# Performance work log

Measured on AMD Instinct MI355X. Metric: run time of the kernel, lower is better.

Reference implementation:

```python
import jax, jax.numpy as jnp
import numpy as np

B = 65536      # batch of (state, action) pairs
DIM_S = 64     # input feature dim
DIM_C = 8      # number of options / experts
H = 256        # hidden width (two hidden layers)


def setup_inputs() -> dict:
    key = jax.random.key(0)
    ks = jax.random.split(key, 7)
    s = 0.05  # small init scale
    st = jax.random.normal(ks[0], (B, DIM_S), dtype=jnp.float32)
    # Batched expert weights: one slice per expert (dim_c experts).
    W1 = jax.random.normal(ks[1], (DIM_C, DIM_S, H), dtype=jnp.float32) * s
    b1 = jax.random.normal(ks[2], (DIM_C, H), dtype=jnp.float32) * s
    W2 = jax.random.normal(ks[3], (DIM_C, H, H), dtype=jnp.float32) * s
    b2 = jax.random.normal(ks[4], (DIM_C, H), dtype=jnp.float32) * s
    W3 = jax.random.normal(ks[5], (DIM_C, H, 1), dtype=jnp.float32) * s
    b3 = jax.random.normal(ks[6], (DIM_C, 1), dtype=jnp.float32) * s
    return {"st": st, "W1": W1, "b1": b1, "W2": W2, "b2": b2,
            "W3": W3, "b3": b3}


def reference(st, W1, b1, W2, b2, W3, b3):
    # Equivalent of torch.stack([m(st) for m in self.discriminator], dim=1):
    # every expert MLP (dim_s -> H -> H -> 1, ReLU) applied to the same st,
    # expressed as batched GEMMs over the expert axis c.
    h = jax.nn.relu(jnp.einsum('bs,csh->bch', st, W1) + b1[None])   # [B, C, H]
    h = jax.nn.relu(jnp.einsum('bch,chk->bck', h, W2) + b2[None])   # [B, C, H]
    d = jnp.einsum('bch,cho->bco', h, W3) + b3[None]                # [B, C, 1]
    return d
```

## Files before the change

kernel.cpp:

```cpp
#include <hip/hip_runtime.h>
#include <hip/hip_bf16.h>

typedef __bf16 bf16x8 __attribute__((ext_vector_type(8)));
typedef float  f32x4  __attribute__((ext_vector_type(4)));

static constexpr int S  = 64;
static constexpr int C  = 8;
static constexpr int HD = 256;

__device__ __forceinline__ unsigned short f2bf(float f) {
  __hip_bfloat16 b = __float2bfloat16(f);
  unsigned short u;
  __builtin_memcpy(&u, &b, 2);
  return u;
}

__device__ __forceinline__ void gl2lds16(const void* g, void* l) {
  __builtin_amdgcn_global_load_lds(
      (const __attribute__((address_space(1))) unsigned int*)g,
      (__attribute__((address_space(3))) unsigned int*)l, 16, 0, 0);
}

__global__ __launch_bounds__(256) void prep_weights(
    const float* __restrict__ W1, const float* __restrict__ W2,
    unsigned short* __restrict__ W1T, unsigned short* __restrict__ W2T)
{
  __shared__ float tile[32][33];
  const int tid = threadIdx.x, cl = tid & 31, r0 = tid >> 5;
  const int b = blockIdx.x;
  if (b < 512) {
    const int c = b >> 6, t = b & 63, kt = t >> 3, nt = t & 7;
    const float* src = W2 + c * 65536;
    #pragma unroll
    for (int i = 0; i < 4; ++i) {
      int r = r0 + 8 * i;
      tile[r][cl] = src[(kt * 32 + r) * 256 + nt * 32 + cl];
    }
    __syncthreads();
    unsigned short* dst = W2T + c * 65536;
    #pragma unroll
    for (int i = 0; i < 4; ++i) {
      int r = r0 + 8 * i;
      dst[(nt * 32 + r) * 256 + kt * 32 + cl] = f2bf(tile[cl][r]);
    }
  } else {
    const int bb = b - 512;
    const int c = bb >> 4, t = bb & 15, st2 = t >> 3, ht = t & 7;
    const float* src = W1 + c * 16384;
    #pragma unroll
    for (int i = 0; i < 4; ++i) {
      int r = r0 + 8 * i;
      tile[r][cl] = src[(st2 * 32 + r) * 256 + ht * 32 + cl];
    }
    __syncthreads();
    unsigned short* dst = W1T + c * 16384;
    #pragma unroll
    for (int i = 0; i < 4; ++i) {
      int r = r0 + 8 * i;
      dst[(ht * 32 + r) * 64 + st2 * 32 + cl] = f2bf(tile[cl][r]);
    }
  }
}

__global__ __launch_bounds__(256, 2) void moe_fused(
    const float* __restrict__ st,
    const unsigned short* __restrict__ W1T,
    const unsigned short* __restrict__ W2T,
    const float* __restrict__ b1,
    const float* __restrict__ b2,
    const float* __restrict__ W3,
    const float* __restrict__ b3,
    float* __restrict__ out)
{
  constexpr int LDT = 72;

  __shared__ __align__(16) unsigned short sT[256 * LDT];
  __shared__ __align__(16) unsigned short sW2[2 * 32 * 256];

  const int tid  = threadIdx.x;
  const int lane = tid & 63;
  const int wv   = tid >> 6;
  const int l15  = lane & 15;
  const int q    = lane >> 4;
  const int c    = blockIdx.x >> 8;
  const int row0 = (blockIdx.x & 255) * 256;

  const unsigned short* W1c = W1T + c * HD * S;
  const unsigned short* W2c = W2T + c * HD * HD;

  bf16x8 aA[4][2];
  #pragma unroll
  for (int nt = 0; nt < 4; ++nt)
    #pragma unroll
    for (int ks = 0; ks < 2; ++ks) {
      const int row = row0 + wv * 64 + nt * 16 + l15;
      const float4* p = reinterpret_cast<const float4*>(st + (size_t)row * S + ks * 32 + q * 8);
      float4 x = p[0], y = p[1];
      union { bf16x8 v; unsigned short u[8]; } a;
      a.u[0] = f2bf(x.x); a.u[1] = f2bf(x.y); a.u[2] = f2bf(x.z); a.u[3] = f2bf(x.w);
      a.u[4] = f2bf(y.x); a.u[5] = f2bf(y.y); a.u[6] = f2bf(y.z); a.u[7] = f2bf(y.w);
      aA[nt][ks] = a.v;
    }

  float pb2v[8][2], pw3v[8][2], bb3;

  bf16x8 aF[4][4][2];
  #pragma unroll
  for (int cc = 0; cc < 4; ++cc) {
    f32x4 bias[4];
    #pragma unroll
    for (int mt = 0; mt < 4; ++mt)
      bias[mt] = *reinterpret_cast<const f32x4*>(
          b1 + c * HD + cc * 64 + mt * 16 + q * 4);
    bf16x8 aW[2][4];
    #pragma unroll
    for (int ks = 0; ks < 2; ++ks)
      #pragma unroll
      for (int mt = 0; mt < 4; ++mt)
        aW[ks][mt] = *reinterpret_cast<const bf16x8*>(
            W1c + (cc * 64 + mt * 16 + l15) * S + ks * 32 + q * 8);

    if (cc == 3) {
      #pragma unroll
      for (int ch = 0; ch < 8; ++ch)
        #pragma unroll
        for (int ct = 0; ct < 2; ++ct) {
          const int n = ch * 32 + ct * 16 + l15;
          pb2v[ch][ct] = b2[c * HD + n];
          pw3v[ch][ct] = W3[c * HD + n];
        }
      bb3 = b3[c];
      #pragma unroll
      for (int pc = 0; pc < 2; ++pc) {
        unsigned short* buf = sW2 + pc * (32 * 256);
        #pragma unroll
        for (int i = 0; i < 4; ++i) {
          const int b2i = wv * 4 + i;
          const int r   = b2i * 2 + (lane >> 5);
          const int j   = (lane & 31) ^ (r & 7);
          gl2lds16(W2c + (pc * 32 + r) * 256 + j * 8, buf + b2i * 512);
        }
      }
    }

    f32x4 acc[4][4];
    #pragma unroll
    for (int mt = 0; mt < 4; ++mt)
      #pragma unroll
      for (int nt = 0; nt < 4; ++nt)
        acc[mt][nt] = (f32x4){0.f, 0.f, 0.f, 0.f};

    #pragma unroll
    for (int ks = 0; ks < 2; ++ks)
      #pragma unroll
      for (int mt = 0; mt < 4; ++mt)
        #pragma unroll
        for (int nt = 0; nt < 4; ++nt)
          acc[mt][nt] = __builtin_amdgcn_mfma_f32_16x16x32_bf16(
              aW[ks][mt], aA[nt][ks], acc[mt][nt], 0, 0, 0);

    #pragma unroll
    for (int mt = 0; mt < 4; ++mt) {
      #pragma unroll
      for (int nt = 0; nt < 4; ++nt) {
        ushort4 pk;
        float v0 = acc[mt][nt][0] + bias[mt][0]; v0 = v0 > 0.f ? v0 : 0.f;
        float v1 = acc[mt][nt][1] + bias[mt][1]; v1 = v1 > 0.f ? v1 : 0.f;
        float v2 = acc[mt][nt][2] + bias[mt][2]; v2 = v2 > 0.f ? v2 : 0.f;
        float v3 = acc[mt][nt][3] + bias[mt][3]; v3 = v3 > 0.f ? v3 : 0.f;
        pk.x = f2bf(v0); pk.y = f2bf(v1); pk.z = f2bf(v2); pk.w = f2bf(v3);
        *reinterpret_cast<ushort4*>(
            sT + (wv * 64 + nt * 16 + l15) * LDT + mt * 16 + q * 4) = pk;
      }
    }
    __asm__ __volatile__("s_waitcnt lgkmcnt(0)" ::: "memory");
    #pragma unroll
    for (int rt = 0; rt < 4; ++rt)
      #pragma unroll
      for (int k2 = 0; k2 < 2; ++k2)
        aF[cc][rt][k2] = *reinterpret_cast<const bf16x8*>(
            sT + (wv * 64 + rt * 16 + l15) * LDT + k2 * 32 + q * 8);
    __asm__ __volatile__("s_waitcnt lgkmcnt(0)" ::: "memory");
  }

  __syncthreads();

  float dacc[4][4];
  #pragma unroll
  for (int rt = 0; rt < 4; ++rt)
    #pragma unroll
    for (int r = 0; r < 4; ++r) dacc[rt][r] = 0.f;

  #pragma unroll
  for (int ch = 0; ch < 8; ++ch) {
    const unsigned short* buf = sW2 + (ch & 1) * (32 * 256);

    f32x4 acc[4][2];
    #pragma unroll
    for (int rt = 0; rt < 4; ++rt)
      #pragma unroll
      for (int ct = 0; ct < 2; ++ct)
        acc[rt][ct] = (f32x4){0.f, 0.f, 0.f, 0.f};

    #pragma unroll
    for (int ks = 0; ks < 8; ++ks) {
      const int jj = ks * 4 + q;
      const int cc = ks >> 1, k2 = ks & 1;
      #pragma unroll
      for (int ct = 0; ct < 2; ++ct) {
        const int nl = ct * 16 + l15;
        bf16x8 b = *reinterpret_cast<const bf16x8*>(
            buf + nl * 256 + ((jj ^ (l15 & 7)) << 3));
        #pragma unroll
        for (int rt = 0; rt < 4; ++rt)
          acc[rt][ct] = __builtin_amdgcn_mfma_f32_16x16x32_bf16(
              aF[cc][rt][k2], b, acc[rt][ct], 0, 0, 0);
      }
    }

    #pragma unroll
    for (int ct = 0; ct < 2; ++ct) {
      const float bias = pb2v[ch][ct];
      const float w3v  = pw3v[ch][ct];
      #pragma unroll
      for (int rt = 0; rt < 4; ++rt)
        #pragma unroll
        for (int r = 0; r < 4; ++r) {
          float v = acc[rt][ct][r] + bias;
          v = v > 0.f ? v : 0.f;
          dacc[rt][r] += v * w3v;
        }
    }

    __syncthreads();
    if (ch < 6) {
      unsigned short* nbuf = sW2 + (ch & 1) * (32 * 256);
      #pragma unroll
      for (int i = 0; i < 4; ++i) {
        const int b2i = wv * 4 + i;
        const int r   = b2i * 2 + (lane >> 5);
        const int j   = (lane & 31) ^ (r & 7);
        gl2lds16(W2c + ((ch + 2) * 32 + r) * 256 + j * 8, nbuf + b2i * 512);
      }
    }
  }

  #pragma unroll
  for (int rt = 0; rt < 4; ++rt)
    #pragma unroll
    for (int r = 0; r < 4; ++r) {
      float v = dacc[rt][r];
      v += __shfl_xor(v, 1);
      v += __shfl_xor(v, 2);
      v += __shfl_xor(v, 4);
      v += __shfl_xor(v, 8);
      dacc[rt][r] = v;
    }

  if (l15 == 0) {
    const int rbase = row0 + wv * 64 + q * 4;
    #pragma unroll
    for (int rt = 0; rt < 4; ++rt)
      #pragma unroll
      for (int r = 0; r < 4; ++r)
        out[(rbase + rt * 16 + r) * C + c] = dacc[rt][r] + bb3;
  }
}

extern "C" void kernel_launch(void* const* d_in, const int* in_sizes, int n_in,
                              void* d_out, int out_size, void* d_ws, size_t ws_size,
                              hipStream_t stream)
{
  const float* st = (const float*)d_in[0];
  const float* W1 = (const float*)d_in[1];
  const float* b1 = (const float*)d_in[2];
  const float* W2 = (const float*)d_in[3];
  const float* b2 = (const float*)d_in[4];
  const float* W3 = (const float*)d_in[5];
  const float* b3 = (const float*)d_in[6];
  float* out = (float*)d_out;

  unsigned short* W1T = (unsigned short*)d_ws;
  unsigned short* W2T = W1T + C * HD * S;

  prep_weights<<<dim3(640), dim3(256), 0, stream>>>(W1, W2, W1T, W2T);
  moe_fused<<<dim3(2048), dim3(256), 0, stream>>>(st, W1T, W2T, b1, b2, W3, b3, out);
}
```

Before: 189.4 us.

## Stage bf16 input tile in shared memory, reusing the W2 buffer

Input rows are converted to bf16 with coalesced loads, written to an XOR-swizzled LDS buffer that aliases the W2 double buffer, and read back per k-step instead of being held in registers for the whole first layer. W1 fragments are now loaded per k-step, and the b2/W3 loads and the first W2 prefetch move after layer one. This lowers register pressure and improves load coalescing. In exchange the W2 prefetch no longer overlaps layer-one compute, and an extra barrier and LDS round-trip are added.

```diff
diff --git a/kernel.cpp b/kernel.cpp
--- a/kernel.cpp
+++ b/kernel.cpp
@@ -75,7 +75,7 @@
   constexpr int LDT = 72;
 
   __shared__ __align__(16) unsigned short sT[256 * LDT];
-  __shared__ __align__(16) unsigned short sW2[2 * 32 * 256];
+  __shared__ __align__(16) unsigned short sU[2 * 32 * 256];
 
   const int tid  = threadIdx.x;
   const int lane = tid & 63;
@@ -88,21 +88,21 @@
   const unsigned short* W1c = W1T + c * HD * S;
   const unsigned short* W2c = W2T + c * HD * HD;
 
-  bf16x8 aA[4][2];
-  #pragma unroll
-  for (int nt = 0; nt < 4; ++nt)
-    #pragma unroll
-    for (int ks = 0; ks < 2; ++ks) {
-      const int row = row0 + wv * 64 + nt * 16 + l15;
-      const float4* p = reinterpret_cast<const float4*>(st + (size_t)row * S + ks * 32 + q * 8);
+  {
+    #pragma unroll
+    for (int it = 0; it < 8; ++it) {
+      const int r = wv * 64 + it * 8 + (lane >> 3);
+      const int g = lane & 7;
+      const float4* p = reinterpret_cast<const float4*>(
+          st + (size_t)(row0 + r) * S + g * 8);
       float4 x = p[0], y = p[1];
-      union { bf16x8 v; unsigned short u[8]; } a;
-      a.u[0] = f2bf(x.x); a.u[1] = f2bf(x.y); a.u[2] = f2bf(x.z); a.u[3] = f2bf(x.w);
-      a.u[4] = f2bf(y.x); a.u[5] = f2bf(y.y); a.u[6] = f2bf(y.z); a.u[7] = f2bf(y.w);
-      aA[nt][ks] = a.v;
-    }
-
-  float pb2v[8][2], pw3v[8][2], bb3;
+      union { uint4 u4; unsigned short us[8]; } pk;
+      pk.us[0] = f2bf(x.x); pk.us[1] = f2bf(x.y); pk.us[2] = f2bf(x.z); pk.us[3] = f2bf(x.w);
+      pk.us[4] = f2bf(y.x); pk.us[5] = f2bf(y.y); pk.us[6] = f2bf(y.z); pk.us[7] = f2bf(y.w);
+      *reinterpret_cast<uint4*>(sU + r * 64 + ((g ^ (r & 7)) << 3)) = pk.u4;
+    }
+  }
+  __asm__ __volatile__("s_waitcnt lgkmcnt(0)" ::: "memory");
 
   bf16x8 aF[4][4][2];
   #pragma unroll
@@ -112,36 +112,6 @@
     for (int mt = 0; mt < 4; ++mt)
       bias[mt] = *reinterpret_cast<const f32x4*>(
           b1 + c * HD + cc * 64 + mt * 16 + q * 4);
-    bf16x8 aW[2][4];
-    #pragma unroll
-    for (int ks = 0; ks < 2; ++ks)
-      #pragma unroll
-      for (int mt = 0; mt < 4; ++mt)
-        aW[ks][mt] = *reinterpret_cast<const bf16x8*>(
-            W1c + (cc * 64 + mt * 16 + l15) * S + ks * 32 + q * 8);
-
-    if (cc == 3) {
-      #pragma unroll
-      for (int ch = 0; ch < 8; ++ch)
-        #pragma unroll
-        for (int ct = 0; ct < 2; ++ct) {
-          const int n = ch * 32 + ct * 16 + l15;
-          pb2v[ch][ct] = b2[c * HD + n];
-          pw3v[ch][ct] = W3[c * HD + n];
-        }
-      bb3 = b3[c];
-      #pragma unroll
-      for (int pc = 0; pc < 2; ++pc) {
-        unsigned short* buf = sW2 + pc * (32 * 256);
-        #pragma unroll
-        for (int i = 0; i < 4; ++i) {
-          const int b2i = wv * 4 + i;
-          const int r   = b2i * 2 + (lane >> 5);
-          const int j   = (lane & 31) ^ (r & 7);
-          gl2lds16(W2c + (pc * 32 + r) * 256 + j * 8, buf + b2i * 512);
-        }
-      }
-    }
 
     f32x4 acc[4][4];
     #pragma unroll
@@ -151,13 +121,27 @@
         acc[mt][nt] = (f32x4){0.f, 0.f, 0.f, 0.f};
 
     #pragma unroll
-    for (int ks = 0; ks < 2; ++ks)
+    for (int ks = 0; ks < 2; ++ks) {
+      bf16x8 aW[4];
+      #pragma unroll
+      for (int mt = 0; mt < 4; ++mt)
+        aW[mt] = *reinterpret_cast<const bf16x8*>(
+            W1c + (cc * 64 + mt * 16 + l15) * S + ks * 32 + q * 8);
+      bf16x8 bB[4];
+      #pragma unroll
+      for (int nt = 0; nt < 4; ++nt) {
+        const int r = wv * 64 + nt * 16 + l15;
+        const int g = ks * 4 + q;
+        bB[nt] = *reinterpret_cast<const bf16x8*>(
+            sU + r * 64 + ((g ^ (r & 7)) << 3));
+      }
       #pragma unroll
       for (int mt = 0; mt < 4; ++mt)
         #pragma unroll
         for (int nt = 0; nt < 4; ++nt)
           acc[mt][nt] = __builtin_amdgcn_mfma_f32_16x16x32_bf16(
-              aW[ks][mt], aA[nt][ks], acc[mt][nt], 0, 0, 0);
+              aW[mt], bB[nt], acc[mt][nt], 0, 0, 0);
+    }
 
     #pragma unroll
     for (int mt = 0; mt < 4; ++mt) {
@@ -183,8 +167,32 @@
     __asm__ __volatile__("s_waitcnt lgkmcnt(0)" ::: "memory");
   }
 
+  float pb2v[8][2], pw3v[8][2];
+  #pragma unroll
+  for (int ch = 0; ch < 8; ++ch)
+    #pragma unroll
+    for (int ct = 0; ct < 2; ++ct) {
+      const int n = ch * 32 + ct * 16 + l15;
+      pb2v[ch][ct] = b2[c * HD + n];
+      pw3v[ch][ct] = W3[c * HD + n];
+    }
+  const float bb3 = b3[c];
+
   __syncthreads();
 
+  #pragma unroll
+  for (int pc = 0; pc < 2; ++pc) {
+    unsigned short* buf = sU + pc * (32 * 256);
+    #pragma unroll
+    for (int i = 0; i < 4; ++i) {
+      const int b2i = wv * 4 + i;
+      const int r   = b2i * 2 + (lane >> 5);
+      const int j   = (lane & 31) ^ (r & 7);
+      gl2lds16(W2c + (pc * 32 + r) * 256 + j * 8, buf + b2i * 512);
+    }
+  }
+  __syncthreads();
+
   float dacc[4][4];
   #pragma unroll
   for (int rt = 0; rt < 4; ++rt)
@@ -193,7 +201,7 @@
 
   #pragma unroll
   for (int ch = 0; ch < 8; ++ch) {
-    const unsigned short* buf = sW2 + (ch & 1) * (32 * 256);
+    const unsigned short* buf = sU + (ch & 1) * (32 * 256);
 
     f32x4 acc[4][2];
     #pragma unroll
@@ -234,7 +242,7 @@
 
     __syncthreads();
     if (ch < 6) {
-      unsigned short* nbuf = sW2 + (ch & 1) * (32 * 256);
+      unsigned short* nbuf = sU + (ch & 1) * (32 * 256);
       #pragma unroll
       for (int i = 0; i < 4; ++i) {
         const int b2i = wv * 4 + i;
```

Result: faster. 168.1 us (-11.2%).
